# Kernel tuning notes

Hardware: AMD Instinct MI355X
Metric: run time of the kernel (lower is better)

Reference implementation:

```python
import jax, jax.numpy as jnp
import numpy as np
from jax import lax

IC, OC, KS, HYP = 16, 16, 3, 128
BS, D = 4, 96

def setup_inputs() -> dict:
    key = jax.random.key(0)
    ks = jax.random.split(key, 6)
    x = jax.random.normal(ks[0], (BS, IC, D, D, D), dtype=jnp.float32)
    hyp_tensor = jax.random.normal(ks[1], (BS, HYP), dtype=jnp.float32)
    Wk = jax.random.normal(ks[2], (KS*KS*KS*IC*OC, HYP), dtype=jnp.float32) * 0.02
    bk = jax.random.normal(ks[3], (KS*KS*KS*IC*OC,), dtype=jnp.float32) * 0.02
    Wb = jax.random.normal(ks[4], (OC, HYP), dtype=jnp.float32) * 0.02
    bb = jax.random.normal(ks[5], (OC,), dtype=jnp.float32) * 0.02
    return {"x": x, "hyp_tensor": hyp_tensor, "Wk": Wk, "bk": bk, "Wb": Wb, "bb": bb}

def reference(x, hyp_tensor, Wk, bk, Wb, bb):
    bs = x.shape[0]
    # hypernetwork: per-sample kernels and biases (torch Linear: y = h @ W.T + b)
    kernel = (hyp_tensor @ Wk.T + bk).reshape(bs, OC, IC, KS, KS, KS)
    bias = hyp_tensor @ Wb.T + bb                      # [bs, OC]
    # per-sample conv == grouped conv with groups = bs
    xg = x.reshape(1, bs * IC, D, D, D)                # [1, bs*IC, D,H,W]
    kg = kernel.reshape(bs * OC, IC, KS, KS, KS)       # [bs*OC, IC, k,k,k]
    out = lax.conv_general_dilated(
        xg, kg,
        window_strides=(1, 1, 1),
        padding=[(1, 1)] * 3,
        feature_group_count=bs,
        dimension_numbers=("NCDHW", "OIDHW", "NCDHW"),
    )
    out = out.reshape(bs, OC, D, D, D) + bias[:, :, None, None, None]
    return out
```

## Files before the change

### kernel.cpp

```cpp
#include <hip/hip_runtime.h>

#define Dm 96
#define PL (Dm*Dm*Dm)
#define ICn 16
#define OCn 16
#define HYPn 128
#define BSn 4
#define NG 15
#define FRAG_ELEMS (NG*64*8)

#define XP 98
#define ROWB (XP*32)
#define PLANEB (XP*ROWB)
#define SAMPB ((size_t)XP*PLANEB)
#define XT_TOTAL ((size_t)4*SAMPB)

typedef float   f32x4  __attribute__((ext_vector_type(4)));
typedef __bf16  bf16x8 __attribute__((ext_vector_type(8)));

__device__ __forceinline__ unsigned short f2bf(float f) {
    unsigned u = __builtin_bit_cast(unsigned, f);
    u = (u + 0x7FFFu + ((u >> 16) & 1u)) >> 16;
    return (unsigned short)u;
}

__global__ __launch_bounds__(256)
void transpose_kernel(const float* __restrict__ x, char* __restrict__ xT)
{
    int blk = blockIdx.x;
    if (blk >= 1536) {
        int idx = blk - 1536;
        int b = idx >> 1, zb = idx & 1;
        char* p = xT + (size_t)b*SAMPB + (size_t)(zb ? 97 : 0)*PLANEB;
        f32x4 z4 = {0.f,0.f,0.f,0.f};
        for (int i = threadIdx.x; i < PLANEB/16; i += 256)
            *(f32x4*)(p + (size_t)i*16) = z4;
        return;
    }
    int yq = blk & 3;
    int z  = (blk >> 2) % Dm;
    int b  = (blk >> 2) / Dm;
    char* xTp = xT + (size_t)b*SAMPB + (size_t)(z+1)*PLANEB;
    const float* xb = x + (size_t)b*ICn*PL + (size_t)z*Dm*Dm;

    for (int t = threadIdx.x; t < 576; t += 256) {
        int q = t % 24, yy = t / 24;
        int y = yq*24 + yy;
        const float* g = xb + y*Dm + 4*q;
        f32x4 ld[16];
#pragma unroll
        for (int ic = 0; ic < 16; ++ic)
            ld[ic] = *(const f32x4*)(g + (size_t)ic*PL);
        char* w = xTp + (size_t)(y+1)*ROWB + (size_t)(1 + 4*q)*32;
#pragma unroll
        for (int xi = 0; xi < 4; ++xi) {
            bf16x8 lo, hi;
#pragma unroll
            for (int ic = 0; ic < 8; ++ic) { lo[ic] = (__bf16)ld[ic][xi]; hi[ic] = (__bf16)ld[8+ic][xi]; }
            *(bf16x8*)(w + xi*32)      = lo;
            *(bf16x8*)(w + xi*32 + 16) = hi;
        }
    }
    bf16x8 z8;
#pragma unroll
    for (int i = 0; i < 8; ++i) z8[i] = (__bf16)0.f;
    for (int t = threadIdx.x; t < 96; t += 256) {
        int half = t & 1, side = (t >> 1) & 1, yy = t >> 2;
        int y = yq*24 + yy;
        *(bf16x8*)(xTp + (size_t)(y+1)*ROWB + (size_t)(side ? 97 : 0)*32 + half*16) = z8;
    }
    if (yq == 0 || yq == 3) {
        char* w0 = xTp + (size_t)(yq == 0 ? 0 : 97)*ROWB;
        for (int t = threadIdx.x; t < XP*2; t += 256)
            *(bf16x8*)(w0 + (size_t)t*16) = z8;
    }
}

__global__ __launch_bounds__(256)
void hyper_frag_kernel(const float* __restrict__ hyp, const float* __restrict__ Wk,
                       const float* __restrict__ bk, unsigned short* __restrict__ kwf)
{
    int t = blockIdx.x * 256 + threadIdx.x;
    if (t >= BSn * FRAG_ELEMS) return;
    int j    = t & 7;
    int lane = (t >> 3) & 63;
    int rest = t >> 9;
    int grp  = rest % NG;
    int b    = rest / NG;
    int oc = lane & 15, hi = lane >> 4;
    int ty = grp / 5, g = grp % 5;
    int cl = hi >> 1;
    int ic = (hi & 1) * 8 + j;
    int c  = 2 * g + cl;
    float acc = 0.f;
    if (c < 9) {
        int tz = c / 3, tx = c % 3;
        int r = (oc * ICn + ic) * 27 + (tz * 9 + ty * 3 + tx);
        const float4* w = (const float4*)(Wk + (long)r * HYPn);
        const float4* h = (const float4*)(hyp + (long)b * HYPn);
        acc = bk[r];
#pragma unroll
        for (int q = 0; q < HYPn / 4; ++q) {
            float4 a = h[q], cc = w[q];
            acc += a.x * cc.x + a.y * cc.y + a.z * cc.z + a.w * cc.w;
        }
    }
    kwf[t] = f2bf(acc);
}

__global__ __launch_bounds__(64)
void hyper_bias_kernel(const float* __restrict__ hyp, const float* __restrict__ Wb,
                       const float* __restrict__ bb, float* __restrict__ bias)
{
    int t = threadIdx.x;
    int b = t >> 4, oc = t & 15;
    const float4* w = (const float4*)(Wb + (long)oc * HYPn);
    const float4* h = (const float4*)(hyp + (long)b * HYPn);
    float acc = bb[oc];
#pragma unroll
    for (int q = 0; q < HYPn / 4; ++q) {
        float4 a = h[q], c = w[q];
        acc += a.x * c.x + a.y * c.y + a.z * c.z + a.w * c.w;
    }
    bias[t] = acc;
}

#define ZT 4
#define YT 8
#define XT 16
#define ZL 6
#define YL 10
#define XL 18
#define SSTR 32
#define SPN (ZL*YL*XL)
#define LPTS 1088
#define LDSB (LPTS*SSTR)
#define NDMA 34
#define NT 4
#define ZCH (ZT*NT)

__device__ constexpr int coff(int c) {
    return ((c / 3) * YL * XL + (c % 3)) * SSTR;
}

__device__ __forceinline__ void dma_tile(const char* org, char* buf,
                                         const unsigned* goff, int wz, int lane)
{
#pragma unroll
    for (int m = 0; m < 9; ++m) {
        if (wz + 4*m < NDMA) {
            int i = wz + 4*m;
            __builtin_amdgcn_global_load_lds(
                (const __attribute__((address_space(1))) unsigned int*)(org + goff[m]),
                (__attribute__((address_space(3))) unsigned int*)(buf + i*1024 + lane*16),
                16, 0, 0);
        }
    }
}

__global__ __launch_bounds__(256, 2)
void conv_dma_kernel(const char* __restrict__ xT, const unsigned short* __restrict__ kwf,
                     const float* __restrict__ bias, float* __restrict__ out)
{
    __shared__ __align__(16) char smem[2*LDSB];

    const int NB = BSn * 6 * 12 * 6;
    int raw = blockIdx.x;
    int u = (raw & 7) * (NB/8) + (raw >> 3);

    int tx = u % 6;  u /= 6;
    int ty = u % 12; u /= 12;
    int zc = u % 6;
    int b  = u / 6;
    int x0 = tx*XT, y0 = ty*YT, zbase = zc*ZCH;

    int tid  = threadIdx.x;
    int lane = tid & 63;
    int wz   = tid >> 6;

    const unsigned short* kwb = kwf + (long)b * FRAG_ELEMS;
    f32x4 afr[NG];
#pragma unroll
    for (int grp = 0; grp < NG; ++grp) {
        afr[grp] = *(const f32x4*)(kwb + (grp * 64 + lane) * 8);
        asm volatile("" : "+v"(afr[grp]));
    }

    unsigned goff[9];
#pragma unroll
    for (int m = 0; m < 9; ++m) {
        int i = wz + 4*m;
        if (i >= NDMA) i = NDMA - 1;
        int flat = i*64 + lane;
        int p = flat >> 1;  if (p > 1079) p = 1079;
        int half = flat & 1;
        int lz = p / (YL*XL), r = p % (YL*XL), ly = r / XL, lx = r % XL;
        goff[m] = (unsigned)(lz*PLANEB + ly*ROWB + lx*32 + half*16);
    }

    int n   = lane & 15;
    int hi  = lane >> 4;
    int cl  = hi >> 1;
    int ich = hi & 1;

    int addr_g[5];
#pragma unroll
    for (int g = 0; g < 5; ++g) {
        int c = 2 * g + cl;
        if (c > 8) c = 8;
        addr_g[g] = ((wz * YL) * XL + n) * SSTR + ich * 16 + coff(c);
    }

    float4 bv = *(const float4*)(bias + b * OCn + hi * 4);

    const char* xsamp = xT + (size_t)b*SAMPB + (size_t)y0*ROWB + (size_t)x0*32;

    char* buf0 = smem;
    char* buf1 = smem + LDSB;

    dma_tile(xsamp + (size_t)zbase*PLANEB, buf0, goff, wz, lane);
    __syncthreads();

#pragma unroll
    for (int t = 0; t < NT; ++t) {
        char* cur = (t & 1) ? buf1 : buf0;
        char* nxt = (t & 1) ? buf0 : buf1;
        int ztile = zbase + t*ZT;

        if (t + 1 < NT)
            dma_tile(xsamp + (size_t)(ztile + ZT)*PLANEB, nxt, goff, wz, lane);

        f32x4 acc[YT];
#pragma unroll
        for (int yy = 0; yy < YT; ++yy) acc[yy] = (f32x4){0.f,0.f,0.f,0.f};

#pragma unroll
        for (int p = 0; p < YL; ++p) {
            bf16x8 F[5];
#pragma unroll
            for (int g = 0; g < 5; ++g)
                F[g] = *(const bf16x8*)(cur + addr_g[g] + p * (XL * SSTR));
#pragma unroll
            for (int tyk = 0; tyk < 3; ++tyk) {
                int yy = p - tyk;
                if (yy >= 0 && yy < YT) {
#pragma unroll
                    for (int g = 0; g < 5; ++g)
                        acc[yy] = __builtin_amdgcn_mfma_f32_16x16x32_bf16(
                            __builtin_bit_cast(bf16x8, afr[tyk * 5 + g]), F[g], acc[yy], 0, 0, 0);
                }
            }
        }

        int zo = ztile + wz;
#pragma unroll
        for (int yy = 0; yy < YT; ++yy) {
            int yo = y0 + yy;
            long obase = ((((long)b * OCn + hi * 4) * Dm + zo) * Dm + yo) * Dm + x0 + n;
#pragma unroll
            for (int r = 0; r < 4; ++r)
                out[obase + (long)r * PL] = acc[yy][r] + ((const float*)&bv)[r];
        }

        if (t + 1 < NT) {
            asm volatile("s_waitcnt vmcnt(0)" ::: "memory");
            __syncthreads();
        }
    }
}

__global__ __launch_bounds__(256, 4)
void conv_fb_kernel(const float* __restrict__ x, const unsigned short* __restrict__ kwf,
                    const float* __restrict__ bias, float* __restrict__ out)
{
    __shared__ __align__(16) char smem[SPN*SSTR];

    const int NXT = Dm / XT, NYT = Dm / YT, NZT = Dm / ZT;
    int raw = blockIdx.x;
    int bid = (raw & 7) * ((BSn * NXT * NYT * NZT) / 8) + (raw >> 3);

    int txi = bid % NXT; bid /= NXT;
    int tyi = bid % NYT; bid /= NYT;
    int tzi = bid % NZT;
    int b   = bid / NZT;
    int x0 = txi * XT, y0 = tyi * YT, z0 = tzi * ZT;

    int tid  = threadIdx.x;
    int lane = tid & 63;
    int wz   = tid >> 6;

    const float* xb = x + (long)b * ICn * PL;

    for (int t = tid; t < 480; t += 256) {
        int xq  = t & 3;
        int ich = (t >> 2) & 1;
        int row = t >> 3;
        int ly = row % YL, lz = row / YL;
        int gz = z0 - 1 + lz, gy = y0 - 1 + ly;
        int gx = x0 + 4 * xq;
        bf16x8 v[4];
        if ((unsigned)gz < (unsigned)Dm && (unsigned)gy < (unsigned)Dm) {
            const float* g = xb + (long)(ich * 8) * PL + ((long)gz * Dm + gy) * Dm + gx;
#pragma unroll
            for (int q = 0; q < 8; ++q) {
                f32x4 p = *(const f32x4*)(g + (long)q * PL);
                v[0][q] = (__bf16)p.x; v[1][q] = (__bf16)p.y;
                v[2][q] = (__bf16)p.z; v[3][q] = (__bf16)p.w;
            }
        } else {
#pragma unroll
            for (int xi = 0; xi < 4; ++xi)
#pragma unroll
                for (int q = 0; q < 8; ++q) v[xi][q] = (__bf16)0.f;
        }
        int sp = (lz * YL + ly) * XL + (1 + 4 * xq);
#pragma unroll
        for (int xi = 0; xi < 4; ++xi)
            *(bf16x8*)(smem + (sp + xi) * SSTR + ich * 16) = v[xi];
    }
    for (int t = tid; t < 240; t += 256) {
        int s   = t & 1;
        int ich = (t >> 1) & 1;
        int row = t >> 2;
        int ly = row % YL, lz = row / YL;
        int gz = z0 - 1 + lz, gy = y0 - 1 + ly;
        int lx = s ? (XL - 1) : 0;
        int gx = x0 - 1 + lx;
        bf16x8 v;
        if ((unsigned)gz < (unsigned)Dm && (unsigned)gy < (unsigned)Dm &&
            (unsigned)gx < (unsigned)Dm) {
            const float* g = xb + (long)(ich * 8) * PL + ((long)gz * Dm + gy) * Dm + gx;
#pragma unroll
            for (int q = 0; q < 8; ++q) v[q] = (__bf16)g[(long)q * PL];
        } else {
#pragma unroll
            for (int q = 0; q < 8; ++q) v[q] = (__bf16)0.f;
        }
        int sp = (lz * YL + ly) * XL + lx;
        *(bf16x8*)(smem + sp * SSTR + ich * 16) = v;
    }

    const unsigned short* kwb = kwf + (long)b * FRAG_ELEMS;
    f32x4 afr[NG];
#pragma unroll
    for (int grp = 0; grp < NG; ++grp) {
        afr[grp] = *(const f32x4*)(kwb + (grp * 64 + lane) * 8);
        asm volatile("" : "+v"(afr[grp]));
    }

    __syncthreads();

    int n   = lane & 15;
    int hi  = lane >> 4;
    int cl  = hi >> 1;
    int ich = hi & 1;

    int addr_g[5];
#pragma unroll
    for (int g = 0; g < 5; ++g) {
        int c = 2 * g + cl;
        if (c > 8) c = 8;
        addr_g[g] = ((wz * YL) * XL + n) * SSTR + ich * 16 + coff(c);
    }

    f32x4 acc[YT];
#pragma unroll
    for (int yy = 0; yy < YT; ++yy) acc[yy] = (f32x4){0.f, 0.f, 0.f, 0.f};

#pragma unroll
    for (int p = 0; p < YL; ++p) {
        bf16x8 F[5];
#pragma unroll
        for (int g = 0; g < 5; ++g)
            F[g] = *(const bf16x8*)(smem + addr_g[g] + p * (XL * SSTR));
#pragma unroll
        for (int tyk = 0; tyk < 3; ++tyk) {
            int yy = p - tyk;
            if (yy >= 0 && yy < YT) {
#pragma unroll
                for (int g = 0; g < 5; ++g)
                    acc[yy] = __builtin_amdgcn_mfma_f32_16x16x32_bf16(
                        __builtin_bit_cast(bf16x8, afr[tyk * 5 + g]), F[g], acc[yy], 0, 0, 0);
            }
        }
    }

    float4 bv = *(const float4*)(bias + b * OCn + hi * 4);
    int zo = z0 + wz;
#pragma unroll
    for (int yy = 0; yy < YT; ++yy) {
        int yo = y0 + yy;
        long obase = ((((long)b * OCn + hi * 4) * Dm + zo) * Dm + yo) * Dm + x0 + n;
#pragma unroll
        for (int r = 0; r < 4; ++r)
            out[obase + (long)r * PL] = acc[yy][r] + ((const float*)&bv)[r];
    }
}

extern "C" void kernel_launch(void* const* d_in, const int* in_sizes, int n_in,
                              void* d_out, int out_size, void* d_ws, size_t ws_size,
                              hipStream_t stream)
{
    const float* x   = (const float*)d_in[0];
    const float* hyp = (const float*)d_in[1];
    const float* Wk  = (const float*)d_in[2];
    const float* bk  = (const float*)d_in[3];
    const float* Wb  = (const float*)d_in[4];
    const float* bb  = (const float*)d_in[5];
    float* out = (float*)d_out;

    const size_t need = XT_TOTAL + 61440 + 256;
    if (ws_size >= need) {
        char* xT = (char*)d_ws;
        unsigned short* kwf = (unsigned short*)(xT + XT_TOTAL);
        float* biasp = (float*)(xT + XT_TOTAL + 61440);

        hipLaunchKernelGGL(transpose_kernel, dim3(1544), dim3(256), 0, stream, x, xT);
        hipLaunchKernelGGL(hyper_frag_kernel, dim3((BSn * FRAG_ELEMS) / 256), dim3(256), 0, stream,
                           hyp, Wk, bk, kwf);
        hipLaunchKernelGGL(hyper_bias_kernel, dim3(1), dim3(64), 0, stream,
                           hyp, Wb, bb, biasp);
        hipLaunchKernelGGL(conv_dma_kernel, dim3(BSn * 6 * 12 * 6), dim3(256), 0, stream,
                           xT, kwf, biasp, out);
    } else {
        unsigned short* kwf = (unsigned short*)d_ws;
        float* biasp = (float*)((char*)d_ws + (size_t)BSn * FRAG_ELEMS * 2);

        hipLaunchKernelGGL(hyper_frag_kernel, dim3((BSn * FRAG_ELEMS) / 256), dim3(256), 0, stream,
                           hyp, Wk, bk, kwf);
        hipLaunchKernelGGL(hyper_bias_kernel, dim3(1), dim3(64), 0, stream,
                           hyp, Wb, bb, biasp);
        hipLaunchKernelGGL(conv_fb_kernel, dim3(BSn * 6 * 12 * 24), dim3(256), 0, stream,
                           x, kwf, biasp, out);
    }
}
```

Baseline: 205.2 us.

## Fuse prep kernels, lengthen per-block z chunk, and relax DMA wait

Merges the transpose, hypernetwork kernel-fragment and bias kernels into one prep launch, which removes launch overhead. The transpose now splits each point's channels across two threads to raise parallelism. The conv kernel processes six z-tiles per block instead of four, giving fewer blocks and more reuse of the resident weight fragments. It also replaces the full vmcnt(0) wait and __syncthreads with a partial vmcnt wait plus a raw barrier and sched_barriers, so that outstanding output stores do not stall the pipeline. Fewer blocks (1152) may lower occupancy balance across CUs.

```diff
diff --git a/kernel.cpp b/kernel.cpp
--- a/kernel.cpp
+++ b/kernel.cpp
@@ -25,104 +25,105 @@
 }
 
 __global__ __launch_bounds__(256)
-void transpose_kernel(const float* __restrict__ x, char* __restrict__ xT)
+void prep_kernel(const float* __restrict__ x, char* __restrict__ xT,
+                 const float* __restrict__ hyp, const float* __restrict__ Wk,
+                 const float* __restrict__ bk, unsigned short* __restrict__ kwf,
+                 const float* __restrict__ Wb, const float* __restrict__ bb,
+                 float* __restrict__ bias, int boff)
 {
-    int blk = blockIdx.x;
-    if (blk >= 1536) {
+    int blk = blockIdx.x + boff;
+    int tid = threadIdx.x;
+
+    if (blk < 1536) {
+        int yq = blk & 3;
+        int z  = (blk >> 2) % Dm;
+        int b  = (blk >> 2) / Dm;
+        char* xTp = xT + (size_t)b*SAMPB + (size_t)(z+1)*PLANEB;
+        const float* xb = x + (size_t)b*ICn*PL + (size_t)z*Dm*Dm;
+
+        for (int t = tid; t < 1152; t += 256) {
+            int ich = t & 1;
+            int r   = t >> 1;
+            int q = r % 24, yy = r / 24;
+            int y = yq*24 + yy;
+            const float* g = xb + (size_t)(ich*8)*PL + y*Dm + 4*q;
+            f32x4 ld[8];
+#pragma unroll
+            for (int ic = 0; ic < 8; ++ic)
+                ld[ic] = *(const f32x4*)(g + (size_t)ic*PL);
+            char* w = xTp + (size_t)(y+1)*ROWB + (size_t)(1 + 4*q)*32 + ich*16;
+#pragma unroll
+            for (int xi = 0; xi < 4; ++xi) {
+                bf16x8 v;
+#pragma unroll
+                for (int e = 0; e < 8; ++e) v[e] = (__bf16)ld[e][xi];
+                *(bf16x8*)(w + xi*32) = v;
+            }
+        }
+        bf16x8 z8;
+#pragma unroll
+        for (int i = 0; i < 8; ++i) z8[i] = (__bf16)0.f;
+        for (int t = tid; t < 96; t += 256) {
+            int half = t & 1, side = (t >> 1) & 1, yy = t >> 2;
+            int y = yq*24 + yy;
+            *(bf16x8*)(xTp + (size_t)(y+1)*ROWB + (size_t)(side ? 97 : 0)*32 + half*16) = z8;
+        }
+        if (yq == 0 || yq == 3) {
+            char* w0 = xTp + (size_t)(yq == 0 ? 0 : 97)*ROWB;
+            for (int t = tid; t < XP*2; t += 256)
+                *(bf16x8*)(w0 + (size_t)t*16) = z8;
+        }
+        return;
+    }
+    if (blk < 1544) {
         int idx = blk - 1536;
         int b = idx >> 1, zb = idx & 1;
         char* p = xT + (size_t)b*SAMPB + (size_t)(zb ? 97 : 0)*PLANEB;
         f32x4 z4 = {0.f,0.f,0.f,0.f};
-        for (int i = threadIdx.x; i < PLANEB/16; i += 256)
+        for (int i = tid; i < PLANEB/16; i += 256)
             *(f32x4*)(p + (size_t)i*16) = z4;
         return;
     }
-    int yq = blk & 3;
-    int z  = (blk >> 2) % Dm;
-    int b  = (blk >> 2) / Dm;
-    char* xTp = xT + (size_t)b*SAMPB + (size_t)(z+1)*PLANEB;
-    const float* xb = x + (size_t)b*ICn*PL + (size_t)z*Dm*Dm;
-
-    for (int t = threadIdx.x; t < 576; t += 256) {
-        int q = t % 24, yy = t / 24;
-        int y = yq*24 + yy;
-        const float* g = xb + y*Dm + 4*q;
-        f32x4 ld[16];
-#pragma unroll
-        for (int ic = 0; ic < 16; ++ic)
-            ld[ic] = *(const f32x4*)(g + (size_t)ic*PL);
-        char* w = xTp + (size_t)(y+1)*ROWB + (size_t)(1 + 4*q)*32;
-#pragma unroll
-        for (int xi = 0; xi < 4; ++xi) {
-            bf16x8 lo, hi;
-#pragma unroll
-            for (int ic = 0; ic < 8; ++ic) { lo[ic] = (__bf16)ld[ic][xi]; hi[ic] = (__bf16)ld[8+ic][xi]; }
-            *(bf16x8*)(w + xi*32)      = lo;
-            *(bf16x8*)(w + xi*32 + 16) = hi;
-        }
-    }
-    bf16x8 z8;
-#pragma unroll
-    for (int i = 0; i < 8; ++i) z8[i] = (__bf16)0.f;
-    for (int t = threadIdx.x; t < 96; t += 256) {
-        int half = t & 1, side = (t >> 1) & 1, yy = t >> 2;
-        int y = yq*24 + yy;
-        *(bf16x8*)(xTp + (size_t)(y+1)*ROWB + (size_t)(side ? 97 : 0)*32 + half*16) = z8;
-    }
-    if (yq == 0 || yq == 3) {
-        char* w0 = xTp + (size_t)(yq == 0 ? 0 : 97)*ROWB;
-        for (int t = threadIdx.x; t < XP*2; t += 256)
-            *(bf16x8*)(w0 + (size_t)t*16) = z8;
-    }
-}
-
-__global__ __launch_bounds__(256)
-void hyper_frag_kernel(const float* __restrict__ hyp, const float* __restrict__ Wk,
-                       const float* __restrict__ bk, unsigned short* __restrict__ kwf)
-{
-    int t = blockIdx.x * 256 + threadIdx.x;
-    if (t >= BSn * FRAG_ELEMS) return;
-    int j    = t & 7;
-    int lane = (t >> 3) & 63;
-    int rest = t >> 9;
-    int grp  = rest % NG;
-    int b    = rest / NG;
-    int oc = lane & 15, hi = lane >> 4;
-    int ty = grp / 5, g = grp % 5;
-    int cl = hi >> 1;
-    int ic = (hi & 1) * 8 + j;
-    int c  = 2 * g + cl;
-    float acc = 0.f;
-    if (c < 9) {
-        int tz = c / 3, tx = c % 3;
-        int r = (oc * ICn + ic) * 27 + (tz * 9 + ty * 3 + tx);
-        const float4* w = (const float4*)(Wk + (long)r * HYPn);
+    if (blk < 1664) {
+        int t = (blk - 1544) * 256 + tid;
+        int j    = t & 7;
+        int lane = (t >> 3) & 63;
+        int rest = t >> 9;
+        int grp  = rest % NG;
+        int b    = rest / NG;
+        int oc = lane & 15, hi = lane >> 4;
+        int ty = grp / 5, g = grp % 5;
+        int cl = hi >> 1;
+        int ic = (hi & 1) * 8 + j;
+        int c  = 2 * g + cl;
+        float acc = 0.f;
+        if (c < 9) {
+            int tz = c / 3, tx = c % 3;
+            int r = (oc * ICn + ic) * 27 + (tz * 9 + ty * 3 + tx);
+            const float4* w = (const float4*)(Wk + (long)r * HYPn);
+            const float4* h = (const float4*)(hyp + (long)b * HYPn);
+            acc = bk[r];
+#pragma unroll
+            for (int q = 0; q < HYPn / 4; ++q) {
+                float4 a = h[q], cc = w[q];
+                acc += a.x * cc.x + a.y * cc.y + a.z * cc.z + a.w * cc.w;
+            }
+        }
+        kwf[t] = f2bf(acc);
+        return;
+    }
+    if (tid < 64) {
+        int b = tid >> 4, oc = tid & 15;
+        const float4* w = (const float4*)(Wb + (long)oc * HYPn);
         const float4* h = (const float4*)(hyp + (long)b * HYPn);
-        acc = bk[r];
+        float acc = bb[oc];
 #pragma unroll
         for (int q = 0; q < HYPn / 4; ++q) {
-            float4 a = h[q], cc = w[q];
-            acc += a.x * cc.x + a.y * cc.y + a.z * cc.z + a.w * cc.w;
-        }
-    }
-    kwf[t] = f2bf(acc);
-}
-
-__global__ __launch_bounds__(64)
-void hyper_bias_kernel(const float* __restrict__ hyp, const float* __restrict__ Wb,
-                       const float* __restrict__ bb, float* __restrict__ bias)
-{
-    int t = threadIdx.x;
-    int b = t >> 4, oc = t & 15;
-    const float4* w = (const float4*)(Wb + (long)oc * HYPn);
-    const float4* h = (const float4*)(hyp + (long)b * HYPn);
-    float acc = bb[oc];
-#pragma unroll
-    for (int q = 0; q < HYPn / 4; ++q) {
-        float4 a = h[q], c = w[q];
-        acc += a.x * c.x + a.y * c.y + a.z * c.z + a.w * c.w;
-    }
-    bias[t] = acc;
+            float4 a = h[q], c = w[q];
+            acc += a.x * c.x + a.y * c.y + a.z * c.z + a.w * c.w;
+        }
+        bias[tid] = acc;
+    }
 }
 
 #define ZT 4
@@ -136,7 +137,7 @@
 #define LPTS 1088
 #define LDSB (LPTS*SSTR)
 #define NDMA 34
-#define NT 4
+#define NT 6
 #define ZCH (ZT*NT)
 
 __device__ constexpr int coff(int c) {
@@ -164,14 +165,14 @@
 {
     __shared__ __align__(16) char smem[2*LDSB];
 
-    const int NB = BSn * 6 * 12 * 6;
+    const int NB = BSn * 6 * 12 * 4;
     int raw = blockIdx.x;
     int u = (raw & 7) * (NB/8) + (raw >> 3);
 
     int tx = u % 6;  u /= 6;
     int ty = u % 12; u /= 12;
-    int zc = u % 6;
-    int b  = u / 6;
+    int zc = u % 4;
+    int b  = u / 4;
     int x0 = tx*XT, y0 = ty*YT, zbase = zc*ZCH;
 
     int tid  = threadIdx.x;
@@ -227,8 +228,10 @@
         char* nxt = (t & 1) ? buf0 : buf1;
         int ztile = zbase + t*ZT;
 
-        if (t + 1 < NT)
+        if (t + 1 < NT) {
             dma_tile(xsamp + (size_t)(ztile + ZT)*PLANEB, nxt, goff, wz, lane);
+            __builtin_amdgcn_sched_barrier(0);
+        }
 
         f32x4 acc[YT];
 #pragma unroll
@@ -263,8 +266,9 @@
         }
 
         if (t + 1 < NT) {
-            asm volatile("s_waitcnt vmcnt(0)" ::: "memory");
-            __syncthreads();
+            asm volatile("s_waitcnt vmcnt(32)" ::: "memory");
+            __builtin_amdgcn_s_barrier();
+            __builtin_amdgcn_sched_barrier(0);
         }
     }
 }
@@ -415,21 +419,16 @@
         unsigned short* kwf = (unsigned short*)(xT + XT_TOTAL);
         float* biasp = (float*)(xT + XT_TOTAL + 61440);
 
-        hipLaunchKernelGGL(transpose_kernel, dim3(1544), dim3(256), 0, stream, x, xT);
-        hipLaunchKernelGGL(hyper_frag_kernel, dim3((BSn * FRAG_ELEMS) / 256), dim3(256), 0, stream,
-                           hyp, Wk, bk, kwf);
-        hipLaunchKernelGGL(hyper_bias_kernel, dim3(1), dim3(64), 0, stream,
-                           hyp, Wb, bb, biasp);
-        hipLaunchKernelGGL(conv_dma_kernel, dim3(BSn * 6 * 12 * 6), dim3(256), 0, stream,
+        hipLaunchKernelGGL(prep_kernel, dim3(1665), dim3(256), 0, stream,
+                           x, xT, hyp, Wk, bk, kwf, Wb, bb, biasp, 0);
+        hipLaunchKernelGGL(conv_dma_kernel, dim3(BSn * 6 * 12 * 4), dim3(256), 0, stream,
                            xT, kwf, biasp, out);
     } else {
         unsigned short* kwf = (unsigned short*)d_ws;
         float* biasp = (float*)((char*)d_ws + (size_t)BSn * FRAG_ELEMS * 2);
 
-        hipLaunchKernelGGL(hyper_frag_kernel, dim3((BSn * FRAG_ELEMS) / 256), dim3(256), 0, stream,
-                           hyp, Wk, bk, kwf);
-        hipLaunchKernelGGL(hyper_bias_kernel, dim3(1), dim3(64), 0, stream,
-                           hyp, Wb, bb, biasp);
+        hipLaunchKernelGGL(prep_kernel, dim3(121), dim3(256), 0, stream,
+                           x, (char*)d_ws, hyp, Wk, bk, kwf, Wb, bb, biasp, 1544);
         hipLaunchKernelGGL(conv_fb_kernel, dim3(BSn * 6 * 12 * 24), dim3(256), 0, stream,
                            x, kwf, biasp, out);
     }
```

Result: faster. 190.1 us (-7.4%).
